# Kernel tuning notes

Hardware: AMD Instinct MI355X
Metric: run time of the kernel (lower is better)

The kernel has to match this reference:

```python
import jax, jax.numpy as jnp
import numpy as np

NEG_SLOPE = 0.2

def gat_layer(x, src, dst, W, a_src, a_dst, num_nodes):
    """PyG-style GATConv. W:[F_in,H*C], a_src/a_dst:[H,C]. Returns [N,H,C]."""
    H, C = a_src.shape
    h = (x @ W).reshape(num_nodes, H, C)                      # [N,H,C]
    e_src = jnp.sum(h * a_src, axis=-1)                       # [N,H]
    e_dst = jnp.sum(h * a_dst, axis=-1)                       # [N,H]
    e = jax.nn.leaky_relu(e_src[src] + e_dst[dst], NEG_SLOPE) # [E,H]
    # segment softmax over incoming edges of each destination node
    m = jax.ops.segment_max(e, dst, num_segments=num_nodes)
    w = jnp.exp(e - m[dst])
    z = jax.ops.segment_sum(w, dst, num_segments=num_nodes)
    alpha = w / (z[dst] + 1e-16)                               # [E,H]
    msg = h[src] * alpha[:, :, None]                           # [E,H,C]
    return jax.ops.segment_sum(msg, dst, num_segments=num_nodes)


def setup_inputs() -> dict:
    key = jax.random.key(0)
    ks = jax.random.split(key, 16)
    N, E, F_IN, HID, A, G = 50000, 800000, 128, 128, 32, 64
    x = jax.random.normal(ks[0], (N, F_IN), dtype=jnp.float32)
    edge_index = jax.random.randint(ks[1], (2, E), 0, N, dtype=jnp.int32)
    batch = jnp.sort(jax.random.randint(ks[2], (N,), 0, G, dtype=jnp.int32))
    s = 0.1
    W1 = jax.random.normal(ks[3], (F_IN, 2 * HID), jnp.float32) * s
    a_src1 = jax.random.normal(ks[4], (2, HID), jnp.float32) * s
    a_dst1 = jax.random.normal(ks[5], (2, HID), jnp.float32) * s
    b1 = jnp.zeros((2 * HID,), jnp.float32)
    W2 = jax.random.normal(ks[6], (2 * HID, HID), jnp.float32) * s
    a_src2 = jax.random.normal(ks[7], (1, HID), jnp.float32) * s
    a_dst2 = jax.random.normal(ks[8], (1, HID), jnp.float32) * s
    b2 = jnp.zeros((HID,), jnp.float32)
    Wp = jax.random.normal(ks[9], (HID, A), jnp.float32) * s
    bp = jnp.zeros((A,), jnp.float32)
    Wv = jax.random.normal(ks[10], (HID, 1), jnp.float32) * s
    bv = jnp.zeros((1,), jnp.float32)
    return {"x": x, "edge_index": edge_index, "batch": batch,
            "W1": W1, "a_src1": a_src1, "a_dst1": a_dst1, "b1": b1,
            "W2": W2, "a_src2": a_src2, "a_dst2": a_dst2, "b2": b2,
            "Wp": Wp, "bp": bp, "Wv": Wv, "bv": bv}


def reference(x, edge_index, batch, W1, a_src1, a_dst1, b1,
              W2, a_src2, a_dst2, b2, Wp, bp, Wv, bv):
    N = x.shape[0]
    G = 64  # number of graphs in the batch
    # add self-loops (PyG GATConv default)
    loop = jnp.arange(N, dtype=edge_index.dtype)
    src = jnp.concatenate([edge_index[0], loop])
    dst = jnp.concatenate([edge_index[1], loop])
    # layer 1: heads=2, concat=True
    h1 = gat_layer(x, src, dst, W1, a_src1, a_dst1, N)        # [N,2,HID]
    h1 = jax.nn.elu(h1.reshape(N, -1) + b1)                   # [N,2*HID]
    # layer 2: heads=1, concat=False (mean over heads = identity for H=1)
    h2 = gat_layer(h1, src, dst, W2, a_src2, a_dst2, N)       # [N,1,HID]
    h2 = jax.nn.elu(h2.reshape(N, -1) + b2)                   # [N,HID]
    # global mean pool over graphs
    sums = jax.ops.segment_sum(h2, batch, num_segments=G)
    cnt = jax.ops.segment_sum(jnp.ones((N,), h2.dtype), batch, num_segments=G)
    x_pool = sums / jnp.maximum(cnt, 1.0)[:, None]            # [G,HID]
    policy_logits = x_pool @ Wp + bp                          # [G,A]
    state_value = x_pool @ Wv + bv                            # [G,1]
    return (policy_logits, state_value)
```

## Files before the change

### kernel.cpp

```cpp
#include <hip/hip_runtime.h>
#include <hip/hip_bf16.h>
#include <cstdint>


typedef __attribute__((ext_vector_type(8))) short bf16x8;
typedef __attribute__((ext_vector_type(4))) float f32x4;

#define NBLK_H 160
#define BSH 6
#define BMSK 63

__device__ __forceinline__ float wave_sum(float v) {
#pragma unroll
    for (int off = 32; off >= 1; off >>= 1) v += __shfl_xor(v, off, 64);
    return v;
}

__device__ __forceinline__ unsigned short f2bf(float f) {
    union { float f; uint32_t u; } c; c.f = f;
    uint32_t u = c.u;
    return (unsigned short)((u + 0x7fffu + ((u >> 16) & 1u)) >> 16);
}

__device__ __forceinline__ float bf2f(unsigned short u) {
    union { uint32_t u; float f; } c; c.u = ((uint32_t)u) << 16;
    return c.f;
}


template <int K, int FOUT>
__device__ __forceinline__ void swizzle_body(const float* __restrict__ W, int ldW, int colOff,
                                             unsigned short* __restrict__ Bsw, int tid) {
    constexpr int CPW = FOUT / 4, NCT = CPW / 16, KST = K / 32;
    if (tid >= K * FOUT / 8) return;
    int lane = tid & 63;
    int rest = tid >> 6;
    int t = rest % KST; rest /= KST;
    int c = rest % NCT; rest /= NCT;
    int cg_ = rest;
    int quad = lane >> 4, lo = lane & 15;
    int col = colOff + cg_ * CPW + c * 16 + lo;
    unsigned short v[8];
#pragma unroll
    for (int j = 0; j < 8; ++j)
        v[j] = f2bf(W[(t * 32 + quad * 8 + j) * ldW + col]);
    ushort4* dst = (ushort4*)(Bsw + (size_t)tid * 8);
    ushort4 o0, o1;
    o0.x = v[0]; o0.y = v[1]; o0.z = v[2]; o0.w = v[3];
    o1.x = v[4]; o1.y = v[5]; o1.z = v[6]; o1.w = v[7];
    dst[0] = o0; dst[1] = o1;
}


__global__ __launch_bounds__(256) void init_kernel(
        const float* __restrict__ W1, const float* __restrict__ W2,
        const float* __restrict__ a_src1, const float* __restrict__ a_dst1,
        unsigned short* __restrict__ B1h0, unsigned short* __restrict__ B1h1,
        unsigned short* __restrict__ B2,
        float* __restrict__ v1s, float* __restrict__ v1d,
        int* __restrict__ zbase, int zn4, int ZB,
        const int* __restrict__ ei, int* __restrict__ hist,
        int E, int ET, int CHUNK, int NB) {
    __shared__ int bins[1024];
    int b = blockIdx.x;
    if (b < 8)        swizzle_body<128, 128>(W1, 256, 0,   B1h0, b * 256 + threadIdx.x);
    else if (b < 16)  swizzle_body<128, 128>(W1, 256, 128, B1h1, (b - 8) * 256 + threadIdx.x);
    else if (b < 32)  swizzle_body<256, 128>(W2, 128, 0,   B2, (b - 16) * 256 + threadIdx.x);
    else if (b == 32) {
        int t = threadIdx.x, h = t >> 7, k = t & 127;
        float vs = 0.f, vd = 0.f;
        for (int c = 0; c < 128; ++c) {
            float w = W1[k * 256 + h * 128 + c];
            vs += w * a_src1[h * 128 + c];
            vd += w * a_dst1[h * 128 + c];
        }
        v1s[h * 128 + k] = vs;
        v1d[h * 128 + k] = vd;
    } else if (b < 33 + ZB) {
        int i = (b - 33) * 256 + threadIdx.x;
        if (i < zn4) ((int4*)zbase)[i] = make_int4(0, 0, 0, 0);
    } else {
        const int blk = b - 33 - ZB;
        for (int t = threadIdx.x; t < NB; t += 256) bins[t] = 0;
        __syncthreads();
        const int start = blk * CHUNK, end = min(ET, start + CHUNK);
        for (int i = start + threadIdx.x; i < end; i += 256) {
            int dst = (i < E) ? ei[E + i] : (i - E);
            atomicAdd(&bins[dst >> BSH], 1);
        }
        __syncthreads();
        for (int t = threadIdx.x; t < NB; t += 256) hist[t * NBLK_H + blk] = bins[t];
    }
}


__global__ __launch_bounds__(256) void scan_attn1(
        int* __restrict__ hist, int* __restrict__ tsum, int M, int TILESH,
        const float* __restrict__ x, const float* __restrict__ v1s,
        const float* __restrict__ v1d, float* __restrict__ es1,
        float* __restrict__ ed1, unsigned short* __restrict__ xbf, int N) {
    __shared__ int buf[256];
    if ((int)blockIdx.x < TILESH) {
        const int t = threadIdx.x;
        const int base = blockIdx.x * 1024 + t * 4;
        int v[4]; int s = 0;
#pragma unroll
        for (int k = 0; k < 4; ++k) { v[k] = (base + k < M) ? hist[base + k] : 0; s += v[k]; }
        buf[t] = s;
        __syncthreads();
#pragma unroll
        for (int off = 1; off < 256; off <<= 1) {
            int xx = (t >= off) ? buf[t - off] : 0;
            __syncthreads();
            buf[t] += xx;
            __syncthreads();
        }
        int run = buf[t] - s;
#pragma unroll
        for (int k = 0; k < 4; ++k) {
            if (base + k < M) hist[base + k] = run;
            run += v[k];
        }
        if (t == 255) tsum[blockIdx.x] = buf[255];
        return;
    }
    int bid = blockIdx.x - TILESH;
    int wid = (bid * 256 + threadIdx.x) >> 6;
    int lane = threadIdx.x & 63;
    if (wid >= N) return;
    float2 xv = *(const float2*)(x + (size_t)wid * 128 + lane * 2);
    float p0s = xv.x * v1s[lane * 2] + xv.y * v1s[lane * 2 + 1];
    float p1s = xv.x * v1s[128 + lane * 2] + xv.y * v1s[128 + lane * 2 + 1];
    float p0d = xv.x * v1d[lane * 2] + xv.y * v1d[lane * 2 + 1];
    float p1d = xv.x * v1d[128 + lane * 2] + xv.y * v1d[128 + lane * 2 + 1];
    p0s = wave_sum(p0s); p1s = wave_sum(p1s);
    p0d = wave_sum(p0d); p1d = wave_sum(p1d);
    if (lane == 0) {
        es1[wid * 2] = p0s; es1[wid * 2 + 1] = p1s;
        ed1[wid * 2] = p0d; ed1[wid * 2 + 1] = p1d;
    }
    ushort2 o; o.x = f2bf(xv.x); o.y = f2bf(xv.y);
    *(ushort2*)(xbf + (size_t)wid * 128 + lane * 2) = o;
}


__global__ __launch_bounds__(256) void part_kernel(const int* __restrict__ ei,
                                                   const int* __restrict__ hist,
                                                   const int* __restrict__ tsum,
                                                   int* __restrict__ bsorted,
                                                   int* __restrict__ segbase,
                                                   int E, int ET, int CHUNK, int NB, int T) {
    __shared__ int sb[256];
    __shared__ int scur[1024];
    const int t = threadIdx.x;
    sb[t] = (t < T) ? tsum[t] : 0;
    __syncthreads();
#pragma unroll
    for (int off = 1; off < 256; off <<= 1) {
        int v = (t >= off) ? sb[t - off] : 0;
        __syncthreads();
        sb[t] += v;
        __syncthreads();
    }
    const int blk = blockIdx.x;
    for (int b = t; b < NB; b += 256) {
        int idx = b * NBLK_H + blk;
        int tile = idx >> 10;
        int v = hist[idx] + (tile ? sb[tile - 1] : 0);
        scur[b] = v;
        if (blk == 0) segbase[b] = v;
    }
    if (blk == 0 && t == 0) segbase[NB] = sb[T - 1];
    __syncthreads();
    const int start = blk * CHUNK, end = min(ET, start + CHUNK);
    for (int i = start + t; i < end; i += 256) {
        int dst = (i < E) ? ei[E + i] : (i - E);
        int src = (i < E) ? ei[i] : dst;
        int pos = atomicAdd(&scur[dst >> BSH], 1);
        bsorted[pos] = (src << BSH) | (dst & BMSK);
    }
}


__global__ __launch_bounds__(256) void bucket_kernel(const int* __restrict__ bsorted,
                                                     const int* __restrict__ segbase,
                                                     const float* __restrict__ es1,
                                                     const float* __restrict__ ed1,
                                                     int* __restrict__ csr_src,
                                                     float2* __restrict__ csr_alpha,
                                                     int* __restrict__ rowptr,
                                                     int N, int NB) {
    __shared__ int cnt[64], excl[64];
    __shared__ float z0[64], z1[64];
    __shared__ float2 edv[64];
    __shared__ int ebuf[3072];
    __shared__ float2 wbuf[3072];
    const int b = blockIdx.x;
    const int gbase = segbase[b], gend = segbase[b + 1];
    const int sz = gend - gbase;
    const int t = threadIdx.x;
    if (b == 0 && t == 0) rowptr[N] = segbase[NB];
    if (t < 64) {
        cnt[t] = 0; z0[t] = 0.f; z1[t] = 0.f;
        int dst = (b << BSH) + t;
        if (dst < N) edv[t] = *(const float2*)(ed1 + dst * 2);
        else edv[t] = make_float2(0.f, 0.f);
    }
    __syncthreads();
    const bool fits = (sz <= 3072);
    for (int i = t; i < sz; i += 256) {
        int p = bsorted[gbase + i];
        int s = p >> BSH, ld = p & BMSK;
        float2 esv = *(const float2*)(es1 + s * 2);
        float e0 = esv.x + edv[ld].x; e0 = (e0 > 0.f) ? e0 : 0.2f * e0;
        float e1 = esv.y + edv[ld].y; e1 = (e1 > 0.f) ? e1 : 0.2f * e1;
        float w0 = __expf(e0), w1 = __expf(e1);
        if (fits) { ebuf[i] = p; wbuf[i] = make_float2(w0, w1); }
        atomicAdd(&z0[ld], w0);
        atomicAdd(&z1[ld], w1);
        atomicAdd(&cnt[ld], 1);
    }
    __syncthreads();
    if (t < 64) excl[t] = cnt[t];
    __syncthreads();
    for (int off = 1; off < 64; off <<= 1) {
        int v = (t < 64 && t >= off) ? excl[t - off] : 0;
        __syncthreads();
        if (t < 64) excl[t] += v;
        __syncthreads();
    }
    if (t < 64) {
        int dst = (b << BSH) + t;
        if (dst < N) rowptr[dst] = gbase + excl[t] - cnt[t];
    }
    __syncthreads();
    if (t < 64) {
        cnt[t] = excl[t] - cnt[t];
        z0[t] = 1.f / (z0[t] + 1e-16f);
        z1[t] = 1.f / (z1[t] + 1e-16f);
    }
    __syncthreads();
    if (fits) {
        for (int i = t; i < sz; i += 256) {
            int p = ebuf[i]; float2 wv = wbuf[i];
            int ld = p & BMSK;
            int pos = atomicAdd(&cnt[ld], 1);
            csr_src[gbase + pos] = p >> BSH;
            csr_alpha[gbase + pos] = make_float2(wv.x * z0[ld], wv.y * z1[ld]);
        }
    } else {
        for (int i = t; i < sz; i += 256) {
            int p = bsorted[gbase + i];
            int s = p >> BSH, ld = p & BMSK;
            float2 esv = *(const float2*)(es1 + s * 2);
            float e0 = esv.x + edv[ld].x; e0 = (e0 > 0.f) ? e0 : 0.2f * e0;
            float e1 = esv.y + edv[ld].y; e1 = (e1 > 0.f) ? e1 : 0.2f * e1;
            float w0 = __expf(e0), w1 = __expf(e1);
            int pos = atomicAdd(&cnt[ld], 1);
            csr_src[gbase + pos] = s;
            csr_alpha[gbase + pos] = make_float2(w0 * z0[ld], w1 * z1[ld]);
        }
    }
}


#define ACC2(U_, WW_, P_, Q_) { float v_;                              \
    v_ = bf2f(U_.x); P_.x += WW_.x * v_; Q_.x += WW_.y * v_;           \
    v_ = bf2f(U_.y); P_.y += WW_.x * v_; Q_.y += WW_.y * v_;           \
    v_ = bf2f(U_.z); P_.z += WW_.x * v_; Q_.z += WW_.y * v_;           \
    v_ = bf2f(U_.w); P_.w += WW_.x * v_; Q_.w += WW_.y * v_; }

__global__ void gat_agg_x(const unsigned short* __restrict__ xbf,
                          const int* __restrict__ rowptr, const int* __restrict__ csr_src,
                          const float2* __restrict__ csr_alpha,
                          unsigned short* __restrict__ aggx, int N, int NPAD) {
    __shared__ int    s_lds[4][2][32];
    __shared__ float2 a_lds[4][2][32];
    const int wave = threadIdx.x >> 6, lane = threadIdx.x & 63;
    const int g = lane >> 5, c = lane & 31;
    const int node = (blockIdx.x * 4 + wave) * 2 + g;
    if (node >= N) return;
    const int rs = rowptr[node], re = rowptr[node + 1];
    float4 p = {0.f, 0.f, 0.f, 0.f}, q = {0.f, 0.f, 0.f, 0.f};
    for (int i = rs; i < re; i += 32) {
        const int cnt = min(re - i, 32);
        if (c < cnt) {
            s_lds[wave][g][c] = csr_src[i + c];
            a_lds[wave][g][c] = csr_alpha[i + c];
        }
        int k = 0;
        for (; k + 7 < cnt; k += 8) {
            int s0 = s_lds[wave][g][k + 0], s1 = s_lds[wave][g][k + 1];
            int s2 = s_lds[wave][g][k + 2], s3 = s_lds[wave][g][k + 3];
            int s4 = s_lds[wave][g][k + 4], s5 = s_lds[wave][g][k + 5];
            int s6 = s_lds[wave][g][k + 6], s7 = s_lds[wave][g][k + 7];
            float2 a0 = a_lds[wave][g][k + 0], a1 = a_lds[wave][g][k + 1];
            float2 a2 = a_lds[wave][g][k + 2], a3 = a_lds[wave][g][k + 3];
            float2 a4 = a_lds[wave][g][k + 4], a5 = a_lds[wave][g][k + 5];
            float2 a6 = a_lds[wave][g][k + 6], a7 = a_lds[wave][g][k + 7];
            ushort4 u0 = *(const ushort4*)(xbf + (size_t)s0 * 128 + c * 4);
            ushort4 u1 = *(const ushort4*)(xbf + (size_t)s1 * 128 + c * 4);
            ushort4 u2 = *(const ushort4*)(xbf + (size_t)s2 * 128 + c * 4);
            ushort4 u3 = *(const ushort4*)(xbf + (size_t)s3 * 128 + c * 4);
            ushort4 u4 = *(const ushort4*)(xbf + (size_t)s4 * 128 + c * 4);
            ushort4 u5 = *(const ushort4*)(xbf + (size_t)s5 * 128 + c * 4);
            ushort4 u6 = *(const ushort4*)(xbf + (size_t)s6 * 128 + c * 4);
            ushort4 u7 = *(const ushort4*)(xbf + (size_t)s7 * 128 + c * 4);
            ACC2(u0, a0, p, q);
            ACC2(u1, a1, p, q);
            ACC2(u2, a2, p, q);
            ACC2(u3, a3, p, q);
            ACC2(u4, a4, p, q);
            ACC2(u5, a5, p, q);
            ACC2(u6, a6, p, q);
            ACC2(u7, a7, p, q);
        }
        for (; k < cnt; ++k) {
            int s0 = s_lds[wave][g][k];
            float2 a0 = a_lds[wave][g][k];
            ushort4 u0 = *(const ushort4*)(xbf + (size_t)s0 * 128 + c * 4);
            ACC2(u0, a0, p, q);
        }
    }
    ushort4 o;
    o.x = f2bf(p.x); o.y = f2bf(p.y); o.z = f2bf(p.z); o.w = f2bf(p.w);
    *(ushort4*)(aggx + (size_t)node * 128 + c * 4) = o;
    o.x = f2bf(q.x); o.y = f2bf(q.y); o.z = f2bf(q.z); o.w = f2bf(q.w);
    *(ushort4*)(aggx + (size_t)NPAD * 128 + (size_t)node * 128 + c * 4) = o;
}


__global__ __launch_bounds__(256) void gemm12_fused(
        const unsigned short* __restrict__ Abase,
        const unsigned short* __restrict__ B1h0, const unsigned short* __restrict__ B1h1,
        const unsigned short* __restrict__ B2sw,
        const float* __restrict__ b1,
        const float* __restrict__ a_src, const float* __restrict__ a_dst,
        float* __restrict__ es, float* __restrict__ ed,
        unsigned short* __restrict__ C, int N, int NPAD) {
    __shared__ unsigned short h1t[64][264];
    __shared__ float lds_ps[4][64];
    __shared__ float lds_pd[4][64];
    const int tid = threadIdx.x;
    const int wave = tid >> 6, lane = tid & 63;
    const int quad = lane >> 4, lo = lane & 15;
    const int n0 = blockIdx.x * 64;

    {
        const int head = wave >> 1, wh = wave & 1;
        const unsigned short* A = Abase + (size_t)head * NPAD * 128;
        const bf16x8* Bp = (const bf16x8*)(head ? B1h1 : B1h0);
        bf16x8 bf[4][4];
#pragma unroll
        for (int c = 0; c < 4; ++c)
#pragma unroll
            for (int t = 0; t < 4; ++t)
                bf[c][t] = Bp[((wh * 4 + c) * 4 + t) * 64 + lane];
        f32x4 acc[4][4];
#pragma unroll
        for (int r = 0; r < 4; ++r)
#pragma unroll
            for (int c = 0; c < 4; ++c) acc[r][c] = (f32x4){0.f, 0.f, 0.f, 0.f};
#pragma unroll
        for (int r = 0; r < 4; ++r) {
            const unsigned short* Ar = A + (size_t)(n0 + r * 16 + lo) * 128 + quad * 8;
#pragma unroll
            for (int t = 0; t < 4; ++t) {
                bf16x8 af = *(const bf16x8*)(Ar + t * 32);
#pragma unroll
                for (int c = 0; c < 4; ++c)
                    acc[r][c] = __builtin_amdgcn_mfma_f32_16x16x32_bf16(af, bf[c][t],
                                                                       acc[r][c], 0, 0, 0);
            }
        }
#pragma unroll
        for (int r = 0; r < 4; ++r) {
            int rl = r * 16 + quad * 4;
#pragma unroll
            for (int c = 0; c < 4; ++c) {
                int col = head * 128 + wh * 64 + c * 16 + lo;
                float bv = b1[col];
#pragma unroll
                for (int j = 0; j < 4; ++j) {
                    float v = acc[r][c][j] + bv;
                    v = (v > 0.f) ? v : __expf(v) - 1.f;
                    h1t[rl + j][col] = f2bf(v);
                }
            }
        }
    }
    __syncthreads();

    bf16x8 bf2[2][8];
    {
        const bf16x8* Bp2 = (const bf16x8*)B2sw;
#pragma unroll
        for (int c = 0; c < 2; ++c)
#pragma unroll
            for (int t = 0; t < 8; ++t)
                bf2[c][t] = Bp2[((wave * 2 + c) * 8 + t) * 64 + lane];
    }
    f32x4 acc2[4][2];
#pragma unroll
    for (int r = 0; r < 4; ++r)
#pragma unroll
        for (int c = 0; c < 2; ++c) acc2[r][c] = (f32x4){0.f, 0.f, 0.f, 0.f};
#pragma unroll
    for (int r = 0; r < 4; ++r) {
        const unsigned short* Ar = &h1t[r * 16 + lo][quad * 8];
#pragma unroll
        for (int t = 0; t < 8; ++t) {
            bf16x8 af = *(const bf16x8*)(Ar + t * 32);
#pragma unroll
            for (int c = 0; c < 2; ++c)
                acc2[r][c] = __builtin_amdgcn_mfma_f32_16x16x32_bf16(af, bf2[c][t],
                                                                    acc2[r][c], 0, 0, 0);
        }
    }
    const int c0 = wave * 32;
#pragma unroll
    for (int r = 0; r < 4; ++r) {
        int row = n0 + r * 16 + quad * 4;
#pragma unroll
        for (int c = 0; c < 2; ++c) {
            int col = c0 + c * 16 + lo;
#pragma unroll
            for (int j = 0; j < 4; ++j)
                if (row + j < N) C[(size_t)(row + j) * 128 + col] = f2bf(acc2[r][c][j]);
        }
    }
    float asv[2], adv[2];
#pragma unroll
    for (int c = 0; c < 2; ++c) {
        int col = c0 + c * 16 + lo;
        asv[c] = a_src[col];
        adv[c] = a_dst[col];
    }
#pragma unroll
    for (int r = 0; r < 4; ++r) {
#pragma unroll
        for (int j = 0; j < 4; ++j) {
            float ps = 0.f, pd = 0.f;
#pragma unroll
            for (int c = 0; c < 2; ++c) { ps += acc2[r][c][j] * asv[c]; pd += acc2[r][c][j] * adv[c]; }
#pragma unroll
            for (int off = 1; off <= 8; off <<= 1) {
                ps += __shfl_xor(ps, off, 64);
                pd += __shfl_xor(pd, off, 64);
            }
            if (lo == 0) {
                int row_l = r * 16 + quad * 4 + j;
                lds_ps[wave][row_l] = ps;
                lds_pd[wave][row_l] = pd;
            }
        }
    }
    __syncthreads();
    if (tid < 64) {
        int row = tid;
        int n = n0 + row;
        if (n < N) {
            es[n] = lds_ps[0][row] + lds_ps[1][row] + lds_ps[2][row] + lds_ps[3][row];
            ed[n] = lds_pd[0][row] + lds_pd[1][row] + lds_pd[2][row] + lds_pd[3][row];
        }
    }
}


__global__ void alpha2_kernel(const int* __restrict__ rowptr, const int* __restrict__ csr_src,
                              const float* __restrict__ es, const float* __restrict__ ed,
                              float* __restrict__ csr_a2, int N) {
    int wid = (blockIdx.x * blockDim.x + threadIdx.x) >> 6;
    int lane = threadIdx.x & 63;
    if (wid >= N) return;
    const int rs = rowptr[wid], re = rowptr[wid + 1];
    const float edn = ed[wid];
    float z = 0.f;
    for (int i = rs; i < re; i += 64) {
        int cnt = min(re - i, 64);
        if (lane < cnt) {
            int s = csr_src[i + lane];
            float e = es[s] + edn;
            e = (e > 0.f) ? e : 0.2f * e;
            float w = __expf(e);
            csr_a2[i + lane] = w;
            z += w;
        }
    }
    z = wave_sum(z);
    const float rz = 1.f / (z + 1e-16f);
    for (int i = rs + lane; i < re; i += 64) csr_a2[i] *= rz;
}


#define ACC1(U_, W_, P_) {                                   \
    P_.x += W_ * bf2f(U_.x); P_.y += W_ * bf2f(U_.y);        \
    P_.z += W_ * bf2f(U_.z); P_.w += W_ * bf2f(U_.w); }

__global__ void gat_agg_h1(const unsigned short* __restrict__ Hpre,
                           const int* __restrict__ rowptr, const int* __restrict__ csr_src,
                           const float* __restrict__ csr_a2,
                           const float* __restrict__ bias, unsigned short* __restrict__ out,
                           int N) {
    __shared__ int   s_lds[4][2][32];
    __shared__ float a_lds[4][2][32];
    const int wave = threadIdx.x >> 6, lane = threadIdx.x & 63;
    const int g = lane >> 5, c = lane & 31;
    const int node = (blockIdx.x * 4 + wave) * 2 + g;
    if (node >= N) return;
    const int rs = rowptr[node], re = rowptr[node + 1];
    float4 p = {0.f, 0.f, 0.f, 0.f};
    for (int i = rs; i < re; i += 32) {
        const int cnt = min(re - i, 32);
        if (c < cnt) {
            s_lds[wave][g][c] = csr_src[i + c];
            a_lds[wave][g][c] = csr_a2[i + c];
        }
        int k = 0;
        for (; k + 7 < cnt; k += 8) {
            int s0 = s_lds[wave][g][k + 0], s1 = s_lds[wave][g][k + 1];
            int s2 = s_lds[wave][g][k + 2], s3 = s_lds[wave][g][k + 3];
            int s4 = s_lds[wave][g][k + 4], s5 = s_lds[wave][g][k + 5];
            int s6 = s_lds[wave][g][k + 6], s7 = s_lds[wave][g][k + 7];
            float a0 = a_lds[wave][g][k + 0], a1 = a_lds[wave][g][k + 1];
            float a2 = a_lds[wave][g][k + 2], a3 = a_lds[wave][g][k + 3];
            float a4 = a_lds[wave][g][k + 4], a5 = a_lds[wave][g][k + 5];
            float a6 = a_lds[wave][g][k + 6], a7 = a_lds[wave][g][k + 7];
            ushort4 u0 = *(const ushort4*)(Hpre + (size_t)s0 * 128 + c * 4);
            ushort4 u1 = *(const ushort4*)(Hpre + (size_t)s1 * 128 + c * 4);
            ushort4 u2 = *(const ushort4*)(Hpre + (size_t)s2 * 128 + c * 4);
            ushort4 u3 = *(const ushort4*)(Hpre + (size_t)s3 * 128 + c * 4);
            ushort4 u4 = *(const ushort4*)(Hpre + (size_t)s4 * 128 + c * 4);
            ushort4 u5 = *(const ushort4*)(Hpre + (size_t)s5 * 128 + c * 4);
            ushort4 u6 = *(const ushort4*)(Hpre + (size_t)s6 * 128 + c * 4);
            ushort4 u7 = *(const ushort4*)(Hpre + (size_t)s7 * 128 + c * 4);
            ACC1(u0, a0, p);
            ACC1(u1, a1, p);
            ACC1(u2, a2, p);
            ACC1(u3, a3, p);
            ACC1(u4, a4, p);
            ACC1(u5, a5, p);
            ACC1(u6, a6, p);
            ACC1(u7, a7, p);
        }
        for (; k < cnt; ++k) {
            int s0 = s_lds[wave][g][k];
            float a0 = a_lds[wave][g][k];
            ushort4 u0 = *(const ushort4*)(Hpre + (size_t)s0 * 128 + c * 4);
            ACC1(u0, a0, p);
        }
    }
    float4 bv = ((const float4*)bias)[c];
    float ox = p.x + bv.x, oy = p.y + bv.y, oz = p.z + bv.z, ow = p.w + bv.w;
    ox = (ox > 0.f) ? ox : __expf(ox) - 1.f;
    oy = (oy > 0.f) ? oy : __expf(oy) - 1.f;
    oz = (oz > 0.f) ? oz : __expf(oz) - 1.f;
    ow = (ow > 0.f) ? ow : __expf(ow) - 1.f;
    ushort4 o;
    o.x = f2bf(ox); o.y = f2bf(oy); o.z = f2bf(oz); o.w = f2bf(ow);
    *(ushort4*)(out + (size_t)node * 128 + c * 4) = o;
}


#define PCHUNK 256

__global__ __launch_bounds__(256) void pool_partial(const unsigned short* __restrict__ h2,
                                                    const int* __restrict__ batch,
                                                    float* __restrict__ xsum,
                                                    int* __restrict__ cnt, int N) {
    const int base = blockIdx.x * PCHUNK;
    const int rg = threadIdx.x >> 6;
    const int c2 = threadIdx.x & 63;
    float ax = 0.f, ay = 0.f;
    int gcur = -1, run = 0;
    for (int r = rg; r < PCHUNK; r += 4) {
        int i = base + r;
        if (i >= N) break;
        int g = batch[i];
        if (g != gcur) {
            if (gcur >= 0) {
                atomicAdd(&xsum[gcur * 128 + c2 * 2 + 0], ax);
                atomicAdd(&xsum[gcur * 128 + c2 * 2 + 1], ay);
                if (c2 == 0) atomicAdd(&cnt[gcur], run);
            }
            gcur = g; ax = 0.f; ay = 0.f; run = 0;
        }
        ushort2 u = *(const ushort2*)(h2 + (size_t)i * 128 + c2 * 2);
        ax += bf2f(u.x); ay += bf2f(u.y);
        run += 1;
    }
    if (gcur >= 0) {
        atomicAdd(&xsum[gcur * 128 + c2 * 2 + 0], ax);
        atomicAdd(&xsum[gcur * 128 + c2 * 2 + 1], ay);
        if (c2 == 0) atomicAdd(&cnt[gcur], run);
    }
}


__global__ void head_kernel(const float* __restrict__ xsum, const int* __restrict__ cnt,
                            const float* __restrict__ Wp, const float* __restrict__ bp,
                            const float* __restrict__ Wv, const float* __restrict__ bv,
                            float* __restrict__ out) {
    int g = blockIdx.x, t = threadIdx.x;
    __shared__ float p[128];
    float inv = 1.f / fmaxf((float)cnt[g], 1.f);
    p[t] = xsum[g * 128 + t] * inv;
    p[t + 64] = xsum[g * 128 + t + 64] * inv;
    __syncthreads();
    if (t < 32) {
        float acc = bp[t];
        for (int k = 0; k < 128; ++k) acc += p[k] * Wp[k * 32 + t];
        out[g * 32 + t] = acc;
    } else if (t == 32) {
        float acc = bv[0];
        for (int k = 0; k < 128; ++k) acc += p[k] * Wv[k];
        out[64 * 32 + g] = acc;
    }
}


extern "C" void kernel_launch(void* const* d_in, const int* in_sizes, int n_in,
                              void* d_out, int out_size, void* d_ws, size_t ws_size,
                              hipStream_t stream) {
    const float* x      = (const float*)d_in[0];
    const int*   ei     = (const int*)d_in[1];
    const int*   batch  = (const int*)d_in[2];
    const float* W1     = (const float*)d_in[3];
    const float* a_src1 = (const float*)d_in[4];
    const float* a_dst1 = (const float*)d_in[5];
    const float* b1     = (const float*)d_in[6];
    const float* W2     = (const float*)d_in[7];
    const float* a_src2 = (const float*)d_in[8];
    const float* a_dst2 = (const float*)d_in[9];
    const float* b2     = (const float*)d_in[10];
    const float* Wp     = (const float*)d_in[11];
    const float* bp     = (const float*)d_in[12];
    const float* Wv     = (const float*)d_in[13];
    const float* bv     = (const float*)d_in[14];

    const int N  = in_sizes[0] / 128;
    const int E  = in_sizes[1] / 2;
    const int ET = E + N;
    const int NPAD = ((N + 63) / 64) * 64;
    const int NBLK = NPAD / 64;
    const int PBLK = (N + PCHUNK - 1) / PCHUNK;
    const int NB = (N + 63) >> BSH;
    const int CHUNK = (ET + NBLK_H - 1) / NBLK_H;
    const int M = NB * NBLK_H;
    const int TILESH = (M + 1023) / 1024;
    const int AB = (N + 3) / 4;
    const int GB = (N + 7) / 8;

    char* ws = (char*)d_ws;
    size_t off = 0;
    auto alloc = [&](size_t bytes) -> void* {
        void* p = ws + off;
        off = (off + bytes + 255) & ~(size_t)255;
        return p;
    };
    unsigned short* xbf   = (unsigned short*)alloc((size_t)NPAD * 128 * 2);
    unsigned short* aggx  = (unsigned short*)alloc((size_t)2 * NPAD * 128 * 2);
    unsigned short* h2pre = (unsigned short*)alloc((size_t)NPAD * 128 * 2);
    unsigned short* h2bf  = (unsigned short*)alloc((size_t)N * 128 * 2);
    unsigned short* w1h0  = (unsigned short*)alloc((size_t)128 * 128 * 2);
    unsigned short* w1h1  = (unsigned short*)alloc((size_t)128 * 128 * 2);
    unsigned short* w2sw  = (unsigned short*)alloc((size_t)256 * 128 * 2);
    float* v1s = (float*)alloc(256 * 4);
    float* v1d = (float*)alloc(256 * 4);
    float* es1 = (float*)alloc((size_t)N * 2 * 4);
    float* ed1 = (float*)alloc((size_t)N * 2 * 4);
    float* es2 = (float*)alloc((size_t)N * 4);
    float* ed2 = (float*)alloc((size_t)N * 4);
    const int ZINTS = 64 * 128 + 64;
    int*   zbase  = (int*)alloc(((size_t)ZINTS + 8) * 4);
    float* xsum   = (float*)zbase;
    int*   cnt    = (int*)(xsum + 64 * 128);
    int*    rowptr    = (int*)alloc((size_t)(N + 1) * 4);
    int*    hist      = (int*)alloc((size_t)M * 4);
    int*    segbase   = (int*)alloc((size_t)(NB + 1) * 4);
    int*    bsorted   = (int*)alloc((size_t)ET * 4);
    int*    csrsrc    = (int*)alloc((size_t)ET * 4);
    float2* csralpha  = (float2*)alloc((size_t)ET * 8);
    float*  csra2     = (float*)alloc((size_t)ET * 4);
    int*    tsum      = (int*)alloc(256 * 4);
    const int zn4 = (ZINTS + 3) / 4;
    const int ZB = (zn4 + 255) / 256;

    init_kernel<<<33 + ZB + NBLK_H, 256, 0, stream>>>(W1, W2, a_src1, a_dst1,
                                                      w1h0, w1h1, w2sw, v1s, v1d,
                                                      zbase, zn4, ZB,
                                                      ei, hist, E, ET, CHUNK, NB);
    scan_attn1<<<TILESH + AB, 256, 0, stream>>>(hist, tsum, M, TILESH,
                                                x, v1s, v1d, es1, ed1, xbf, N);
    part_kernel<<<NBLK_H, 256, 0, stream>>>(ei, hist, tsum, bsorted, segbase,
                                            E, ET, CHUNK, NB, TILESH);
    bucket_kernel<<<NB, 256, 0, stream>>>(bsorted, segbase, es1, ed1,
                                          csrsrc, csralpha, rowptr, N, NB);
    gat_agg_x<<<GB, 256, 0, stream>>>(xbf, rowptr, csrsrc, csralpha, aggx, N, NPAD);
    gemm12_fused<<<NBLK, 256, 0, stream>>>(aggx, w1h0, w1h1, w2sw, b1,
                                           a_src2, a_dst2, es2, ed2, h2pre, N, NPAD);
    alpha2_kernel<<<AB, 256, 0, stream>>>(rowptr, csrsrc, es2, ed2, csra2, N);
    gat_agg_h1<<<GB, 256, 0, stream>>>(h2pre, rowptr, csrsrc, csra2, b2, h2bf, N);
    pool_partial<<<PBLK, 256, 0, stream>>>(h2bf, batch, xsum, cnt, N);
    head_kernel<<<64, 64, 0, stream>>>(xsum, cnt, Wp, bp, Wv, bv, (float*)d_out);
}
```

Measured before the change: 304.9 us.

## Fuse layer-1 aggregation into GEMM kernel and fold alpha2 into layer-2 aggregation

The layer-1 edge aggregation now runs inside the GEMM kernel. Each 64-node block gathers its aggregated rows into LDS instead of writing a global aggx buffer and reading it back. Separately, the alpha2 kernel is removed: gat_agg_h1 computes the softmax normalizer and the edge weights on the fly from es2/ed2, avoiding the csra2 round trip and one launch. The trade-offs are more LDS per block (lower occupancy in the fused kernel), fewer waves doing the gather (NBLK blocks instead of GB), and recomputing exp twice per edge in layer 2.

New measurement: 308.6 us. No clear change (+1.2%).

```diff
diff --git a/kernel.cpp b/kernel.cpp
--- a/kernel.cpp
+++ b/kernel.cpp
@@ -270,119 +270,119 @@
     v_ = bf2f(U_.z); P_.z += WW_.x * v_; Q_.z += WW_.y * v_;           \
     v_ = bf2f(U_.w); P_.w += WW_.x * v_; Q_.w += WW_.y * v_; }
 
-__global__ void gat_agg_x(const unsigned short* __restrict__ xbf,
-                          const int* __restrict__ rowptr, const int* __restrict__ csr_src,
-                          const float2* __restrict__ csr_alpha,
-                          unsigned short* __restrict__ aggx, int N, int NPAD) {
-    __shared__ int    s_lds[4][2][32];
-    __shared__ float2 a_lds[4][2][32];
-    const int wave = threadIdx.x >> 6, lane = threadIdx.x & 63;
-    const int g = lane >> 5, c = lane & 31;
-    const int node = (blockIdx.x * 4 + wave) * 2 + g;
-    if (node >= N) return;
-    const int rs = rowptr[node], re = rowptr[node + 1];
-    float4 p = {0.f, 0.f, 0.f, 0.f}, q = {0.f, 0.f, 0.f, 0.f};
-    for (int i = rs; i < re; i += 32) {
-        const int cnt = min(re - i, 32);
-        if (c < cnt) {
-            s_lds[wave][g][c] = csr_src[i + c];
-            a_lds[wave][g][c] = csr_alpha[i + c];
-        }
-        int k = 0;
-        for (; k + 7 < cnt; k += 8) {
-            int s0 = s_lds[wave][g][k + 0], s1 = s_lds[wave][g][k + 1];
-            int s2 = s_lds[wave][g][k + 2], s3 = s_lds[wave][g][k + 3];
-            int s4 = s_lds[wave][g][k + 4], s5 = s_lds[wave][g][k + 5];
-            int s6 = s_lds[wave][g][k + 6], s7 = s_lds[wave][g][k + 7];
-            float2 a0 = a_lds[wave][g][k + 0], a1 = a_lds[wave][g][k + 1];
-            float2 a2 = a_lds[wave][g][k + 2], a3 = a_lds[wave][g][k + 3];
-            float2 a4 = a_lds[wave][g][k + 4], a5 = a_lds[wave][g][k + 5];
-            float2 a6 = a_lds[wave][g][k + 6], a7 = a_lds[wave][g][k + 7];
-            ushort4 u0 = *(const ushort4*)(xbf + (size_t)s0 * 128 + c * 4);
-            ushort4 u1 = *(const ushort4*)(xbf + (size_t)s1 * 128 + c * 4);
-            ushort4 u2 = *(const ushort4*)(xbf + (size_t)s2 * 128 + c * 4);
-            ushort4 u3 = *(const ushort4*)(xbf + (size_t)s3 * 128 + c * 4);
-            ushort4 u4 = *(const ushort4*)(xbf + (size_t)s4 * 128 + c * 4);
-            ushort4 u5 = *(const ushort4*)(xbf + (size_t)s5 * 128 + c * 4);
-            ushort4 u6 = *(const ushort4*)(xbf + (size_t)s6 * 128 + c * 4);
-            ushort4 u7 = *(const ushort4*)(xbf + (size_t)s7 * 128 + c * 4);
-            ACC2(u0, a0, p, q);
-            ACC2(u1, a1, p, q);
-            ACC2(u2, a2, p, q);
-            ACC2(u3, a3, p, q);
-            ACC2(u4, a4, p, q);
-            ACC2(u5, a5, p, q);
-            ACC2(u6, a6, p, q);
-            ACC2(u7, a7, p, q);
-        }
-        for (; k < cnt; ++k) {
-            int s0 = s_lds[wave][g][k];
-            float2 a0 = a_lds[wave][g][k];
-            ushort4 u0 = *(const ushort4*)(xbf + (size_t)s0 * 128 + c * 4);
-            ACC2(u0, a0, p, q);
-        }
-    }
-    ushort4 o;
-    o.x = f2bf(p.x); o.y = f2bf(p.y); o.z = f2bf(p.z); o.w = f2bf(p.w);
-    *(ushort4*)(aggx + (size_t)node * 128 + c * 4) = o;
-    o.x = f2bf(q.x); o.y = f2bf(q.y); o.z = f2bf(q.z); o.w = f2bf(q.w);
-    *(ushort4*)(aggx + (size_t)NPAD * 128 + (size_t)node * 128 + c * 4) = o;
-}
-
-
-__global__ __launch_bounds__(256) void gemm12_fused(
-        const unsigned short* __restrict__ Abase,
+__global__ __launch_bounds__(256) void agg_gemm12(
+        const unsigned short* __restrict__ xbf,
+        const int* __restrict__ rowptr, const int* __restrict__ csr_src,
+        const float2* __restrict__ csr_alpha,
         const unsigned short* __restrict__ B1h0, const unsigned short* __restrict__ B1h1,
         const unsigned short* __restrict__ B2sw,
         const float* __restrict__ b1,
         const float* __restrict__ a_src, const float* __restrict__ a_dst,
         float* __restrict__ es, float* __restrict__ ed,
-        unsigned short* __restrict__ C, int N, int NPAD) {
+        unsigned short* __restrict__ C, int N) {
+    __shared__ unsigned short at[2][64][136];
     __shared__ unsigned short h1t[64][264];
     __shared__ float lds_ps[4][64];
     __shared__ float lds_pd[4][64];
+    __shared__ int    s_lds[4][2][32];
+    __shared__ float2 a_lds[4][2][32];
     const int tid = threadIdx.x;
     const int wave = tid >> 6, lane = tid & 63;
     const int quad = lane >> 4, lo = lane & 15;
+    const int g = lane >> 5, c = lane & 31;
     const int n0 = blockIdx.x * 64;
+
+    for (int it = 0; it < 8; ++it) {
+        const int row = it * 8 + wave * 2 + g;
+        const int node = n0 + row;
+        float4 p = {0.f, 0.f, 0.f, 0.f}, q = {0.f, 0.f, 0.f, 0.f};
+        if (node < N) {
+            const int rs = rowptr[node], re = rowptr[node + 1];
+            for (int i = rs; i < re; i += 32) {
+                const int cnt = min(re - i, 32);
+                if (c < cnt) {
+                    s_lds[wave][g][c] = csr_src[i + c];
+                    a_lds[wave][g][c] = csr_alpha[i + c];
+                }
+                int k = 0;
+                for (; k + 7 < cnt; k += 8) {
+                    int s0 = s_lds[wave][g][k + 0], s1 = s_lds[wave][g][k + 1];
+                    int s2 = s_lds[wave][g][k + 2], s3 = s_lds[wave][g][k + 3];
+                    int s4 = s_lds[wave][g][k + 4], s5 = s_lds[wave][g][k + 5];
+                    int s6 = s_lds[wave][g][k + 6], s7 = s_lds[wave][g][k + 7];
+                    float2 a0 = a_lds[wave][g][k + 0], a1 = a_lds[wave][g][k + 1];
+                    float2 a2 = a_lds[wave][g][k + 2], a3 = a_lds[wave][g][k + 3];
+                    float2 a4 = a_lds[wave][g][k + 4], a5 = a_lds[wave][g][k + 5];
+                    float2 a6 = a_lds[wave][g][k + 6], a7 = a_lds[wave][g][k + 7];
+                    ushort4 u0 = *(const ushort4*)(xbf + (size_t)s0 * 128 + c * 4);
+                    ushort4 u1 = *(const ushort4*)(xbf + (size_t)s1 * 128 + c * 4);
+                    ushort4 u2 = *(const ushort4*)(xbf + (size_t)s2 * 128 + c * 4);
+                    ushort4 u3 = *(const ushort4*)(xbf + (size_t)s3 * 128 + c * 4);
+                    ushort4 u4 = *(const ushort4*)(xbf + (size_t)s4 * 128 + c * 4);
+                    ushort4 u5 = *(const ushort4*)(xbf + (size_t)s5 * 128 + c * 4);
+                    ushort4 u6 = *(const ushort4*)(xbf + (size_t)s6 * 128 + c * 4);
+                    ushort4 u7 = *(const ushort4*)(xbf + (size_t)s7 * 128 + c * 4);
+                    ACC2(u0, a0, p, q);
+                    ACC2(u1, a1, p, q);
+                    ACC2(u2, a2, p, q);
+                    ACC2(u3, a3, p, q);
+                    ACC2(u4, a4, p, q);
+                    ACC2(u5, a5, p, q);
+                    ACC2(u6, a6, p, q);
+                    ACC2(u7, a7, p, q);
+                }
+                for (; k < cnt; ++k) {
+                    int s0 = s_lds[wave][g][k];
+                    float2 a0 = a_lds[wave][g][k];
+                    ushort4 u0 = *(const ushort4*)(xbf + (size_t)s0 * 128 + c * 4);
+                    ACC2(u0, a0, p, q);
+                }
+            }
+        }
+        ushort4 o;
+        o.x = f2bf(p.x); o.y = f2bf(p.y); o.z = f2bf(p.z); o.w = f2bf(p.w);
+        *(ushort4*)(&at[0][row][c * 4]) = o;
+        o.x = f2bf(q.x); o.y = f2bf(q.y); o.z = f2bf(q.z); o.w = f2bf(q.w);
+        *(ushort4*)(&at[1][row][c * 4]) = o;
+    }
+    __syncthreads();
 
     {
         const int head = wave >> 1, wh = wave & 1;
-        const unsigned short* A = Abase + (size_t)head * NPAD * 128;
         const bf16x8* Bp = (const bf16x8*)(head ? B1h1 : B1h0);
         bf16x8 bf[4][4];
 #pragma unroll
-        for (int c = 0; c < 4; ++c)
+        for (int cc = 0; cc < 4; ++cc)
 #pragma unroll
             for (int t = 0; t < 4; ++t)
-                bf[c][t] = Bp[((wh * 4 + c) * 4 + t) * 64 + lane];
+                bf[cc][t] = Bp[((wh * 4 + cc) * 4 + t) * 64 + lane];
         f32x4 acc[4][4];
 #pragma unroll
         for (int r = 0; r < 4; ++r)
 #pragma unroll
-            for (int c = 0; c < 4; ++c) acc[r][c] = (f32x4){0.f, 0.f, 0.f, 0.f};
+            for (int cc = 0; cc < 4; ++cc) acc[r][cc] = (f32x4){0.f, 0.f, 0.f, 0.f};
 #pragma unroll
         for (int r = 0; r < 4; ++r) {
-            const unsigned short* Ar = A + (size_t)(n0 + r * 16 + lo) * 128 + quad * 8;
+            const unsigned short* Ar = &at[head][r * 16 + lo][quad * 8];
 #pragma unroll
             for (int t = 0; t < 4; ++t) {
                 bf16x8 af = *(const bf16x8*)(Ar + t * 32);
 #pragma unroll
-                for (int c = 0; c < 4; ++c)
-                    acc[r][c] = __builtin_amdgcn_mfma_f32_16x16x32_bf16(af, bf[c][t],
-                                                                       acc[r][c], 0, 0, 0);
+                for (int cc = 0; cc < 4; ++cc)
+                    acc[r][cc] = __builtin_amdgcn_mfma_f32_16x16x32_bf16(af, bf[cc][t],
+                                                                        acc[r][cc], 0, 0, 0);
             }
         }
 #pragma unroll
         for (int r = 0; r < 4; ++r) {
             int rl = r * 16 + quad * 4;
 #pragma unroll
-            for (int c = 0; c < 4; ++c) {
-                int col = head * 128 + wh * 64 + c * 16 + lo;
+            for (int cc = 0; cc < 4; ++cc) {
+                int col = head * 128 + wh * 64 + cc * 16 + lo;
                 float bv = b1[col];
 #pragma unroll
                 for (int j = 0; j < 4; ++j) {
-                    float v = acc[r][c][j] + bv;
+                    float v = acc[r][cc][j] + bv;
                     v = (v > 0.f) ? v : __expf(v) - 1.f;
                     h1t[rl + j][col] = f2bf(v);
                 }
@@ -395,16 +395,16 @@
     {
         const bf16x8* Bp2 = (const bf16x8*)B2sw;
 #pragma unroll
-        for (int c = 0; c < 2; ++c)
+        for (int cc = 0; cc < 2; ++cc)
 #pragma unroll
             for (int t = 0; t < 8; ++t)
-                bf2[c][t] = Bp2[((wave * 2 + c) * 8 + t) * 64 + lane];
+                bf2[cc][t] = Bp2[((wave * 2 + cc) * 8 + t) * 64 + lane];
     }
     f32x4 acc2[4][2];
 #pragma unroll
     for (int r = 0; r < 4; ++r)
 #pragma unroll
-        for (int c = 0; c < 2; ++c) acc2[r][c] = (f32x4){0.f, 0.f, 0.f, 0.f};
+        for (int cc = 0; cc < 2; ++cc) acc2[r][cc] = (f32x4){0.f, 0.f, 0.f, 0.f};
 #pragma unroll
     for (int r = 0; r < 4; ++r) {
         const unsigned short* Ar = &h1t[r * 16 + lo][quad * 8];
@@ -412,9 +412,9 @@
         for (int t = 0; t < 8; ++t) {
             bf16x8 af = *(const bf16x8*)(Ar + t * 32);
 #pragma unroll
-            for (int c = 0; c < 2; ++c)
-                acc2[r][c] = __builtin_amdgcn_mfma_f32_16x16x32_bf16(af, bf2[c][t],
-                                                                    acc2[r][c], 0, 0, 0);
+            for (int cc = 0; cc < 2; ++cc)
+                acc2[r][cc] = __builtin_amdgcn_mfma_f32_16x16x32_bf16(af, bf2[cc][t],
+                                                                     acc2[r][cc], 0, 0, 0);
         }
     }
     const int c0 = wave * 32;
@@ -422,19 +422,19 @@
     for (int r = 0; r < 4; ++r) {
         int row = n0 + r * 16 + quad * 4;
 #pragma unroll
-        for (int c = 0; c < 2; ++c) {
-            int col = c0 + c * 16 + lo;
+        for (int cc = 0; cc < 2; ++cc) {
+            int col = c0 + cc * 16 + lo;
 #pragma unroll
             for (int j = 0; j < 4; ++j)
-                if (row + j < N) C[(size_t)(row + j) * 128 + col] = f2bf(acc2[r][c][j]);
+                if (row + j < N) C[(size_t)(row + j) * 128 + col] = f2bf(acc2[r][cc][j]);
         }
     }
     float asv[2], adv[2];
 #pragma unroll
-    for (int c = 0; c < 2; ++c) {
-        int col = c0 + c * 16 + lo;
-        asv[c] = a_src[col];
-        adv[c] = a_dst[col];
+    for (int cc = 0; cc < 2; ++cc) {
+        int col = c0 + cc * 16 + lo;
+        asv[cc] = a_src[col];
+        adv[cc] = a_dst[col];
     }
 #pragma unroll
     for (int r = 0; r < 4; ++r) {
@@ -442,7 +442,7 @@
         for (int j = 0; j < 4; ++j) {
             float ps = 0.f, pd = 0.f;
 #pragma unroll
-            for (int c = 0; c < 2; ++c) { ps += acc2[r][c][j] * asv[c]; pd += acc2[r][c][j] * adv[c]; }
+            for (int cc = 0; cc < 2; ++cc) { ps += acc2[r][cc][j] * asv[cc]; pd += acc2[r][cc][j] * adv[cc]; }
 #pragma unroll
             for (int off = 1; off <= 8; off <<= 1) {
                 ps += __shfl_xor(ps, off, 64);
@@ -467,39 +467,13 @@
 }
 
 
-__global__ void alpha2_kernel(const int* __restrict__ rowptr, const int* __restrict__ csr_src,
-                              const float* __restrict__ es, const float* __restrict__ ed,
-                              float* __restrict__ csr_a2, int N) {
-    int wid = (blockIdx.x * blockDim.x + threadIdx.x) >> 6;
-    int lane = threadIdx.x & 63;
-    if (wid >= N) return;
-    const int rs = rowptr[wid], re = rowptr[wid + 1];
-    const float edn = ed[wid];
-    float z = 0.f;
-    for (int i = rs; i < re; i += 64) {
-        int cnt = min(re - i, 64);
-        if (lane < cnt) {
-            int s = csr_src[i + lane];
-            float e = es[s] + edn;
-            e = (e > 0.f) ? e : 0.2f * e;
-            float w = __expf(e);
-            csr_a2[i + lane] = w;
-            z += w;
-        }
-    }
-    z = wave_sum(z);
-    const float rz = 1.f / (z + 1e-16f);
-    for (int i = rs + lane; i < re; i += 64) csr_a2[i] *= rz;
-}
-
-
 #define ACC1(U_, W_, P_) {                                   \
     P_.x += W_ * bf2f(U_.x); P_.y += W_ * bf2f(U_.y);        \
     P_.z += W_ * bf2f(U_.z); P_.w += W_ * bf2f(U_.w); }
 
 __global__ void gat_agg_h1(const unsigned short* __restrict__ Hpre,
                            const int* __restrict__ rowptr, const int* __restrict__ csr_src,
-                           const float* __restrict__ csr_a2,
+                           const float* __restrict__ es, const float* __restrict__ ed,
                            const float* __restrict__ bias, unsigned short* __restrict__ out,
                            int N) {
     __shared__ int   s_lds[4][2][32];
@@ -509,12 +483,28 @@
     const int node = (blockIdx.x * 4 + wave) * 2 + g;
     if (node >= N) return;
     const int rs = rowptr[node], re = rowptr[node + 1];
+    const float edn = ed[node];
+    float z = 0.f;
+    for (int i = rs; i < re; i += 32) {
+        if (c < min(re - i, 32)) {
+            int s = csr_src[i + c];
+            float e = es[s] + edn;
+            e = (e > 0.f) ? e : 0.2f * e;
+            z += __expf(e);
+        }
+    }
+#pragma unroll
+    for (int off = 16; off >= 1; off >>= 1) z += __shfl_xor(z, off, 64);
+    const float rz = 1.f / (z + 1e-16f);
     float4 p = {0.f, 0.f, 0.f, 0.f};
     for (int i = rs; i < re; i += 32) {
         const int cnt = min(re - i, 32);
         if (c < cnt) {
-            s_lds[wave][g][c] = csr_src[i + c];
-            a_lds[wave][g][c] = csr_a2[i + c];
+            int s = csr_src[i + c];
+            float e = es[s] + edn;
+            e = (e > 0.f) ? e : 0.2f * e;
+            s_lds[wave][g][c] = s;
+            a_lds[wave][g][c] = __expf(e) * rz;
         }
         int k = 0;
         for (; k + 7 < cnt; k += 8) {
@@ -659,7 +649,6 @@
         return p;
     };
     unsigned short* xbf   = (unsigned short*)alloc((size_t)NPAD * 128 * 2);
-    unsigned short* aggx  = (unsigned short*)alloc((size_t)2 * NPAD * 128 * 2);
     unsigned short* h2pre = (unsigned short*)alloc((size_t)NPAD * 128 * 2);
     unsigned short* h2bf  = (unsigned short*)alloc((size_t)N * 128 * 2);
     unsigned short* w1h0  = (unsigned short*)alloc((size_t)128 * 128 * 2);
@@ -681,7 +670,6 @@
     int*    bsorted   = (int*)alloc((size_t)ET * 4);
     int*    csrsrc    = (int*)alloc((size_t)ET * 4);
     float2* csralpha  = (float2*)alloc((size_t)ET * 8);
-    float*  csra2     = (float*)alloc((size_t)ET * 4);
     int*    tsum      = (int*)alloc(256 * 4);
     const int zn4 = (ZINTS + 3) / 4;
     const int ZB = (zn4 + 255) / 256;
@@ -696,11 +684,10 @@
                                             E, ET, CHUNK, NB, TILESH);
     bucket_kernel<<<NB, 256, 0, stream>>>(bsorted, segbase, es1, ed1,
                                           csrsrc, csralpha, rowptr, N, NB);
-    gat_agg_x<<<GB, 256, 0, stream>>>(xbf, rowptr, csrsrc, csralpha, aggx, N, NPAD);
-    gemm12_fused<<<NBLK, 256, 0, stream>>>(aggx, w1h0, w1h1, w2sw, b1,
-                                           a_src2, a_dst2, es2, ed2, h2pre, N, NPAD);
-    alpha2_kernel<<<AB, 256, 0, stream>>>(rowptr, csrsrc, es2, ed2, csra2, N);
-    gat_agg_h1<<<GB, 256, 0, stream>>>(h2pre, rowptr, csrsrc, csra2, b2, h2bf, N);
+    agg_gemm12<<<NBLK, 256, 0, stream>>>(xbf, rowptr, csrsrc, csralpha,
+                                         w1h0, w1h1, w2sw, b1,
+                                         a_src2, a_dst2, es2, ed2, h2pre, N);
+    gat_agg_h1<<<GB, 256, 0, stream>>>(h2pre, rowptr, csrsrc, es2, ed2, b2, h2bf, N);
     pool_partial<<<PBLK, 256, 0, stream>>>(h2bf, batch, xsum, cnt, N);
     head_kernel<<<64, 64, 0, stream>>>(xsum, cnt, Wp, bp, Wv, bv, (float*)d_out);
 }
```
